# Performance work log

Measured on AMD Instinct MI355X. Metric: run time of the kernel, lower is better.

## Reference

```python
import jax, jax.numpy as jnp
import numpy as np

D = 768; H = 12; HEAD = 6; SD = 64; S1 = SD * (HEAD - 1); S2 = SD * HEAD
HID = 3072; B = 8; N = 1024
SCALE = (D // H) ** -0.5
EPS = 1e-5


def _ln(x, g, b):
    m = jnp.mean(x, axis=-1, keepdims=True)
    v = jnp.var(x, axis=-1, keepdims=True)
    return (x - m) * jax.lax.rsqrt(v + EPS) * g + b


def setup_inputs() -> dict:
    key = jax.random.key(0)
    ks = jax.random.split(key, 20)
    p = lambda k, shape, s=0.02: (jax.random.normal(k, shape, dtype=jnp.float32) * s)
    return {
        "x": jax.random.normal(ks[0], (B, N, D), dtype=jnp.float32),
        # norm1 / norm12 / norm13 (pre-attention split LayerNorms)
        "ln1a_g": jnp.ones((S1,), jnp.float32), "ln1a_b": jnp.zeros((S1,), jnp.float32),
        "ln1b_g": jnp.ones((SD,), jnp.float32), "ln1b_b": jnp.zeros((SD,), jnp.float32),
        "ln1c_g": jnp.ones((D - S2,), jnp.float32), "ln1c_b": jnp.zeros((D - S2,), jnp.float32),
        # norm2 / norm22 / norm23 (pre-MLP split LayerNorms)
        "ln2a_g": jnp.ones((S1,), jnp.float32), "ln2a_b": jnp.zeros((S1,), jnp.float32),
        "ln2b_g": jnp.ones((SD,), jnp.float32), "ln2b_b": jnp.zeros((SD,), jnp.float32),
        "ln2c_g": jnp.ones((D - S2,), jnp.float32), "ln2c_b": jnp.zeros((D - S2,), jnp.float32),
        # attention (qkv has no bias since qkv_bias=False)
        "qkv_w": p(ks[1], (3 * D, D)),
        "proj_w": p(ks[2], (D, D)), "proj_b": jnp.zeros((D,), jnp.float32),
        # mlp
        "fc1_w": p(ks[3], (HID, D)), "fc1_b": jnp.zeros((HID,), jnp.float32),
        "fc2_w": p(ks[4], (D, HID)), "fc2_b": jnp.zeros((D,), jnp.float32),
    }


def _split_norm(x, ga, ba, gb, bb, gc, bc):
    return jnp.concatenate([
        _ln(x[:, :, :S1], ga, ba),
        _ln(x[:, :, S1:S2], gb, bb),
        _ln(x[:, :, S2:], gc, bc),
    ], axis=2)


def _attention(x, qkv_w, proj_w, proj_b):
    Bq, Nq, C = x.shape
    hd = C // H
    qkv = jnp.einsum('bnc,dc->bnd', x, qkv_w)  # [B,N,3C]
    qkv = qkv.reshape(Bq, Nq, 3, H, hd).transpose(2, 0, 3, 1, 4)
    q, k, v = qkv[0], qkv[1], qkv[2]  # [B,H,N,hd]
    attn = jax.nn.softmax(jnp.einsum('bhqd,bhkd->bhqk', q, k) * SCALE, axis=-1)
    y = jnp.einsum('bhqk,bhkd->bhqd', attn, v)  # [B,H,N,hd]
    y = y.transpose(0, 2, 1, 3).reshape(Bq, Nq, C)
    return jnp.einsum('bnc,dc->bnd', y, proj_w) + proj_b


def reference(x, ln1a_g, ln1a_b, ln1b_g, ln1b_b, ln1c_g, ln1c_b,
              ln2a_g, ln2a_b, ln2b_g, ln2b_b, ln2c_g, ln2c_b,
              qkv_w, proj_w, proj_b, fc1_w, fc1_b, fc2_w, fc2_b):
    norm_x = _split_norm(x, ln1a_g, ln1a_b, ln1b_g, ln1b_b, ln1c_g, ln1c_b)
    x = x + _attention(norm_x, qkv_w, proj_w, proj_b)
    norm2_x = _split_norm(x, ln2a_g, ln2a_b, ln2b_g, ln2b_b, ln2c_g, ln2c_b)
    h = jax.nn.gelu(jnp.einsum('bnc,hc->bnh', norm2_x, fc1_w) + fc1_b, approximate=False)
    x = x + (jnp.einsum('bnh,ch->bnc', h, fc2_w) + fc2_b)
    return x
```

## Files before the change

### kernel.cpp

```cpp
#include <hip/hip_runtime.h>
#include <math.h>

#define NTOK 8192
#define DIM 768
#define SEQ 1024
#define NH 12
#define HD 64
#define HID 3072
#define S1V 320
#define S2V 384

typedef unsigned short bfu;
typedef __attribute__((ext_vector_type(8))) short short8;
typedef __attribute__((ext_vector_type(4))) float f32x4;

__device__ __forceinline__ bfu f2bf(float f){
  unsigned int u = __float_as_uint(f);
  u += 0x7FFFu + ((u >> 16) & 1u);
  return (bfu)(u >> 16);
}
__device__ __forceinline__ f32x4 mfma16(short8 a, short8 b, f32x4 c){
  return __builtin_amdgcn_mfma_f32_16x16x32_bf16(a, b, c, 0, 0, 0);
}
__device__ __forceinline__ void gll16(const void* g, void* l){
  __builtin_amdgcn_global_load_lds(
      (const __attribute__((address_space(1))) unsigned int*)g,
      (__attribute__((address_space(3))) unsigned int*)l, 16, 0, 0);
}
__device__ __forceinline__ int swz(int a){ return a ^ (((a >> 7) & 7) << 4); }

__global__ __launch_bounds__(256) void cvt_all(
    const float4* __restrict__ s0, ushort4* __restrict__ d0,
    const float4* __restrict__ s1, ushort4* __restrict__ d1,
    const float4* __restrict__ s2, ushort4* __restrict__ d2,
    const float4* __restrict__ s3, ushort4* __restrict__ d3)
{
  const int total = 1769472;
  for (int i = blockIdx.x * 256 + threadIdx.x; i < total; i += gridDim.x * 256){
    const float4* s; ushort4* d; int j = i;
    if (j < 442368)       { s = s0; d = d0; }
    else if (j < 589824)  { s = s1; d = d1; j -= 442368; }
    else if (j < 1179648) { s = s2; d = d2; j -= 589824; }
    else                  { s = s3; d = d3; j -= 1179648; }
    float4 f = s[j];
    ushort4 o;
    o.x = f2bf(f.x); o.y = f2bf(f.y); o.z = f2bf(f.z); o.w = f2bf(f.w);
    d[j] = o;
  }
}

__global__ __launch_bounds__(256) void ln_split(
    const float* __restrict__ x,
    const float* __restrict__ ga, const float* __restrict__ ba,
    const float* __restrict__ gb, const float* __restrict__ bb2,
    const float* __restrict__ gc, const float* __restrict__ bc,
    bfu* __restrict__ out)
{
  const int row = blockIdx.x, t = threadIdx.x;
  const float* xr = x + (size_t)row * DIM;
  const float e0 = xr[t], e1 = xr[t + 256], e2 = xr[t + 512];
  float s0 = e0, q0 = e0 * e0, s1 = 0.f, q1 = 0.f, s2 = e2, q2 = e2 * e2;
  const int i1 = t + 256;
  if (i1 < S1V)      { s0 += e1; q0 += e1 * e1; }
  else if (i1 < S2V) { s1 += e1; q1 += e1 * e1; }
  else               { s2 += e1; q2 += e1 * e1; }
  float v[6] = {s0, q0, s1, q1, s2, q2};
  #pragma unroll
  for (int k = 0; k < 6; ++k)
    #pragma unroll
    for (int off = 32; off; off >>= 1)
      v[k] += __shfl_xor(v[k], off);
  __shared__ float red[6][4];
  const int lane = t & 63, wave = t >> 6;
  if (lane == 0){
    #pragma unroll
    for (int k = 0; k < 6; ++k) red[k][wave] = v[k];
  }
  __syncthreads();
  float tt[6];
  #pragma unroll
  for (int k = 0; k < 6; ++k) tt[k] = red[k][0] + red[k][1] + red[k][2] + red[k][3];
  const float m0 = tt[0] * (1.f/320.f);
  const float r0 = rsqrtf(tt[1] * (1.f/320.f) - m0*m0 + 1e-5f);
  const float m1 = tt[2] * (1.f/64.f);
  const float r1 = rsqrtf(tt[3] * (1.f/64.f) - m1*m1 + 1e-5f);
  const float m2 = tt[4] * (1.f/384.f);
  const float r2 = rsqrtf(tt[5] * (1.f/384.f) - m2*m2 + 1e-5f);
  bfu* orow = out + (size_t)row * DIM;
  orow[t] = f2bf((e0 - m0) * r0 * ga[t] + ba[t]);
  {
    float ov;
    if (i1 < S1V)      ov = (e1 - m0) * r0 * ga[i1] + ba[i1];
    else if (i1 < S2V) ov = (e1 - m1) * r1 * gb[i1 - S1V] + bb2[i1 - S1V];
    else               ov = (e1 - m2) * r2 * gc[i1 - S2V] + bc[i1 - S2V];
    orow[i1] = f2bf(ov);
  }
  const int i2 = t + 512;
  orow[i2] = f2bf((e2 - m2) * r2 * gc[i2 - S2V] + bc[i2 - S2V]);
}

template<int FM, int FN, int BIAS, int GELU_, int RESID, int OUTF32, int QSC>
__device__ __forceinline__ void gemm_core(
    const bfu* __restrict__ A, const bfu* __restrict__ Bw,
    int N, int K, int ntn,
    const float* __restrict__ bias, const float* __restrict__ resid,
    float* __restrict__ outf, bfu* __restrict__ outb)
{
  constexpr int BM = FM * 32, BN = FN * 32;
  constexpr int ABYTES = BM * 64, BBYTES = BN * 64;
  constexpr int AISS = ABYTES / 4096, BISS = BBYTES / 4096;
  __shared__ __align__(16) char lA_[2][ABYTES];
  __shared__ __align__(16) char lB_[2][BBYTES];
  const int tid = threadIdx.x;
  const int lane = tid & 63;
  const int wave = tid >> 6;
  const int wm = wave >> 1, wn = wave & 1;
  const int r = lane & 15, g = lane >> 4;

  const int nwg = gridDim.x, cpx = nwg >> 3;
  const int sb = (blockIdx.x & 7) * cpx + (blockIdx.x >> 3);
  const int tm = sb / ntn, tn = sb % ntn;
  const size_t ld2 = (size_t)K * 2;

  f32x4 acc[FM][FN];
  #pragma unroll
  for (int i = 0; i < FM; ++i)
    #pragma unroll
    for (int j = 0; j < FN; ++j) acc[i][j] = (f32x4){0.f, 0.f, 0.f, 0.f};

  int PofA[AISS], rowA[AISS], colA[AISS];
  #pragma unroll
  for (int is = 0; is < AISS; ++is){
    const int P = is * 4096 + tid * 16, L = swz(P);
    PofA[is] = P; rowA[is] = L >> 6; colA[is] = L & 63;
  }
  int PofB[BISS], rowB[BISS], colB[BISS];
  #pragma unroll
  for (int is = 0; is < BISS; ++is){
    const int P = is * 4096 + tid * 16, L = swz(P);
    PofB[is] = P; rowB[is] = L >> 6; colB[is] = L & 63;
  }
  const char* Abase = (const char*)A + (size_t)tm * BM * ld2;
  const char* Bbase = (const char*)Bw + (size_t)tn * BN * ld2;

  int offA[FM], offB[FN];
  #pragma unroll
  for (int f = 0; f < FM; ++f) offA[f] = swz((wm * FM * 16 + f * 16 + r) * 64 + g * 16);
  #pragma unroll
  for (int f = 0; f < FN; ++f) offB[f] = swz((wn * FN * 16 + f * 16 + r) * 64 + g * 16);

  const int nk = K >> 5;
  #pragma unroll
  for (int is = 0; is < AISS; ++is)
    gll16(Abase + (size_t)rowA[is] * ld2 + colA[is], &lA_[0][PofA[is]]);
  #pragma unroll
  for (int is = 0; is < BISS; ++is)
    gll16(Bbase + (size_t)rowB[is] * ld2 + colB[is], &lB_[0][PofB[is]]);
  __syncthreads();

  for (int t = 0; t < nk; ++t){
    const int cur = t & 1;
    if (t + 1 < nk){
      const int kb = (t + 1) * 64;
      #pragma unroll
      for (int is = 0; is < AISS; ++is)
        gll16(Abase + (size_t)rowA[is] * ld2 + kb + colA[is], &lA_[cur ^ 1][PofA[is]]);
      #pragma unroll
      for (int is = 0; is < BISS; ++is)
        gll16(Bbase + (size_t)rowB[is] * ld2 + kb + colB[is], &lB_[cur ^ 1][PofB[is]]);
    }
    const char* lA = lA_[cur];
    const char* lB = lB_[cur];
    short8 af[FM], bf[FN];
    #pragma unroll
    for (int f = 0; f < FM; ++f) af[f] = *(const short8*)(lA + offA[f]);
    #pragma unroll
    for (int f = 0; f < FN; ++f) bf[f] = *(const short8*)(lB + offB[f]);
    #pragma unroll
    for (int i = 0; i < FM; ++i)
      #pragma unroll
      for (int j = 0; j < FN; ++j)
        acc[i][j] = mfma16(af[i], bf[j], acc[i][j]);
    __syncthreads();
  }

  const int row0 = tm * BM + wm * FM * 16;
  const int col0 = tn * BN + wn * FN * 16;
  #pragma unroll
  for (int j = 0; j < FN; ++j){
    const int colb = col0 + j * 16 + r;
    const float bi = BIAS ? bias[colb] : 0.f;
    #pragma unroll
    for (int i = 0; i < FM; ++i){
      #pragma unroll
      for (int q = 0; q < 4; ++q){
        const int rowg = row0 + i * 16 + g * 4 + q;
        float v = acc[i][j][q] + bi;
        if (GELU_) v = 0.5f * v * (1.f + erff(v * 0.70710678118654752440f));
        if (QSC && colb < 768) v *= 0.125f;
        const size_t idx = (size_t)rowg * N + colb;
        if (RESID) v += resid[idx];
        if (OUTF32) outf[idx] = v;
        else        outb[idx] = f2bf(v);
      }
    }
  }
}

__global__ __launch_bounds__(256) void gemm_qkv(const bfu* A, const bfu* Bw, bfu* out){
  gemm_core<4,4,0,0,0,0,1>(A, Bw, 2304, 768, 18, nullptr, nullptr, nullptr, out);
}
__global__ __launch_bounds__(256) void gemm_proj(const bfu* A, const bfu* Bw,
                                                 const float* bias, const float* resid, float* out){
  gemm_core<2,4,1,0,1,1,0>(A, Bw, 768, 768, 6, bias, resid, out, nullptr);
}
__global__ __launch_bounds__(256) void gemm_fc1(const bfu* A, const bfu* Bw,
                                                const float* bias, bfu* out){
  gemm_core<4,4,1,1,0,0,0>(A, Bw, 3072, 768, 24, bias, nullptr, nullptr, out);
}
__global__ __launch_bounds__(256) void gemm_fc2(const bfu* A, const bfu* Bw,
                                                const float* bias, float* out){
  gemm_core<2,4,1,0,1,1,0>(A, Bw, 768, 3072, 6, bias, out, out, nullptr);
}

__global__ __launch_bounds__(256) void vtrans(const bfu* __restrict__ qkv, bfu* __restrict__ vt){
  __shared__ bfu tile[64][66];
  const int bh = blockIdx.x, kt = blockIdx.y;
  const int b = bh / NH, h = bh - b * NH;
  const int tid = threadIdx.x;
  const int tr = tid >> 5;
  const int tc = (tid & 31) * 2;
  #pragma unroll
  for (int pass = 0; pass < 8; ++pass){
    const int k = pass * 8 + tr;
    const bfu* src = qkv + (size_t)(b * SEQ + kt * 64 + k) * 2304 + 1536 + h * 64 + tc;
    tile[k][tc] = src[0]; tile[k][tc + 1] = src[1];
  }
  __syncthreads();
  #pragma unroll
  for (int pass = 0; pass < 8; ++pass){
    const int d = pass * 8 + tr;
    bfu* dst = vt + ((size_t)bh * 64 + d) * SEQ + kt * 64 + tc;
    dst[0] = tile[tc][d]; dst[1] = tile[tc + 1][d];
  }
}

__global__ __launch_bounds__(512) void attn2(
    const bfu* __restrict__ qkv, const bfu* __restrict__ vt, bfu* __restrict__ y)
{
  __shared__ __align__(16) char kbuf[2][8192];
  __shared__ __align__(16) char vbuf[2][8192];
  __shared__ __align__(16) char plds_all[8][2048];
  const int tid = threadIdx.x, lane = tid & 63, wave = tid >> 6;
  char* plds = plds_all[wave];
  const int blk = blockIdx.x;
  const int bh = blk >> 3, q128 = blk & 7;
  const int b = bh / NH, h = bh - b * NH;
  const int r = lane & 15, g = lane >> 4;

  const bfu* qbase = qkv + (size_t)(b * SEQ + q128 * 128 + wave * 16 + r) * 2304 + h * 64;
  const short8 qf0 = *(const short8*)(qbase + g * 8);
  const short8 qf1 = *(const short8*)(qbase + 32 + g * 8);

  const int P = tid * 16;
  const int Ls = swz(P);
  const int srow = Ls >> 7, scol = Ls & 127;
  const char* kg = (const char*)(qkv + (size_t)(b * SEQ) * 2304 + 768 + h * 64)
                   + (size_t)srow * 4608 + scol;
  const char* vg = (const char*)(vt + (size_t)bh * 64 * SEQ)
                   + (size_t)srow * 2048 + scol;

  int off[4][2];
  #pragma unroll
  for (int f = 0; f < 4; ++f){
    off[f][0] = swz((f * 16 + r) * 128 + g * 16);
    off[f][1] = swz((f * 16 + r) * 128 + 64 + g * 16);
  }

  float m_[4], l_[4];
  f32x4 yacc[4];
  #pragma unroll
  for (int i = 0; i < 4; ++i){ m_[i] = -1e30f; l_[i] = 0.f; yacc[i] = (f32x4){0.f,0.f,0.f,0.f}; }

  gll16(kg, &kbuf[0][P]);
  gll16(vg, &vbuf[0][P]);
  __syncthreads();

  for (int kt = 0; kt < 16; ++kt){
    const int cur = kt & 1;
    if (kt + 1 < 16){
      gll16(kg + (size_t)(kt + 1) * 294912, &kbuf[cur ^ 1][P]);
      gll16(vg + (kt + 1) * 128, &vbuf[cur ^ 1][P]);
    }
    const char* lK = kbuf[cur];
    const char* lV = vbuf[cur];

    f32x4 s[4];
    #pragma unroll
    for (int c = 0; c < 4; ++c){
      const short8 kf0 = *(const short8*)(lK + off[c][0]);
      const short8 kf1 = *(const short8*)(lK + off[c][1]);
      s[c] = (f32x4){0.f, 0.f, 0.f, 0.f};
      s[c] = mfma16(qf0, kf0, s[c]);
      s[c] = mfma16(qf1, kf1, s[c]);
    }
    float pm[4];
    #pragma unroll
    for (int q = 0; q < 4; ++q)
      pm[q] = fmaxf(fmaxf(s[0][q], s[1][q]), fmaxf(s[2][q], s[3][q]));
    #pragma unroll
    for (int q = 0; q < 4; ++q)
      #pragma unroll
      for (int o = 1; o < 16; o <<= 1)
        pm[q] = fmaxf(pm[q], __shfl_xor(pm[q], o));
    float rs[4];
    #pragma unroll
    for (int q = 0; q < 4; ++q){
      const float mn = fmaxf(m_[q], pm[q]);
      const float al = __expf(m_[q] - mn);
      m_[q] = mn;
      l_[q] *= al;
      #pragma unroll
      for (int f = 0; f < 4; ++f) yacc[f][q] *= al;
      float acc = 0.f;
      #pragma unroll
      for (int c = 0; c < 4; ++c){
        const float p = __expf(s[c][q] - mn);
        s[c][q] = p;
        acc += p;
      }
      rs[q] = acc;
    }
    #pragma unroll
    for (int q = 0; q < 4; ++q){
      #pragma unroll
      for (int o = 1; o < 16; o <<= 1)
        rs[q] += __shfl_xor(rs[q], o);
      l_[q] += rs[q];
    }
    #pragma unroll
    for (int c = 0; c < 4; ++c)
      #pragma unroll
      for (int q = 0; q < 4; ++q){
        const int a = swz((g * 4 + q) * 128 + (c * 16 + r) * 2);
        *(bfu*)&plds[a] = f2bf(s[c][q]);
      }
    short8 pa[2];
    #pragma unroll
    for (int ks = 0; ks < 2; ++ks)
      pa[ks] = *(const short8*)&plds[swz(r * 128 + ks * 64 + g * 16)];
    #pragma unroll
    for (int f = 0; f < 4; ++f){
      const short8 vf0 = *(const short8*)(lV + off[f][0]);
      const short8 vf1 = *(const short8*)(lV + off[f][1]);
      yacc[f] = mfma16(pa[0], vf0, yacc[f]);
      yacc[f] = mfma16(pa[1], vf1, yacc[f]);
    }
    __syncthreads();
  }

  bfu* yb = y + (size_t)(b * SEQ + q128 * 128 + wave * 16) * DIM + h * 64;
  #pragma unroll
  for (int f = 0; f < 4; ++f)
    #pragma unroll
    for (int q = 0; q < 4; ++q)
      yb[(size_t)(g * 4 + q) * DIM + f * 16 + r] = f2bf(yacc[f][q] / l_[q]);
}

extern "C" void kernel_launch(void* const* d_in, const int* in_sizes, int n_in,
                              void* d_out, int out_size, void* d_ws, size_t ws_size,
                              hipStream_t stream) {
  const float* x      = (const float*)d_in[0];
  const float* ln1ag  = (const float*)d_in[1];
  const float* ln1ab  = (const float*)d_in[2];
  const float* ln1bg  = (const float*)d_in[3];
  const float* ln1bb  = (const float*)d_in[4];
  const float* ln1cg  = (const float*)d_in[5];
  const float* ln1cb  = (const float*)d_in[6];
  const float* ln2ag  = (const float*)d_in[7];
  const float* ln2ab  = (const float*)d_in[8];
  const float* ln2bg  = (const float*)d_in[9];
  const float* ln2bb  = (const float*)d_in[10];
  const float* ln2cg  = (const float*)d_in[11];
  const float* ln2cb  = (const float*)d_in[12];
  const float* qkv_w  = (const float*)d_in[13];
  const float* proj_w = (const float*)d_in[14];
  const float* proj_b = (const float*)d_in[15];
  const float* fc1_w  = (const float*)d_in[16];
  const float* fc1_b  = (const float*)d_in[17];
  const float* fc2_w  = (const float*)d_in[18];
  const float* fc2_b  = (const float*)d_in[19];
  float* outp = (float*)d_out;

  char* ws = (char*)d_ws;
  bfu* wqkv   = (bfu*)(ws + 0);
  bfu* wproj  = (bfu*)(ws + 3538944);
  bfu* wfc1   = (bfu*)(ws + 4718592);
  bfu* wfc2   = (bfu*)(ws + 9437184);
  bfu* lnbuf  = (bfu*)(ws + 14155776);
  bfu* ybuf   = (bfu*)(ws + 26738688);
  bfu* qkvbuf = (bfu*)(ws + 39321600);
  bfu* vtbuf  = (bfu*)(ws + 77070336);
  bfu* hbuf   = qkvbuf;

  cvt_all<<<2048, 256, 0, stream>>>((const float4*)qkv_w,  (ushort4*)wqkv,
                                    (const float4*)proj_w, (ushort4*)wproj,
                                    (const float4*)fc1_w,  (ushort4*)wfc1,
                                    (const float4*)fc2_w,  (ushort4*)wfc2);

  ln_split<<<NTOK, 256, 0, stream>>>(x, ln1ag, ln1ab, ln1bg, ln1bb, ln1cg, ln1cb, lnbuf);
  gemm_qkv<<<1152, 256, 0, stream>>>(lnbuf, wqkv, qkvbuf);
  vtrans<<<dim3(96,16), 256, 0, stream>>>(qkvbuf, vtbuf);
  attn2<<<768, 512, 0, stream>>>(qkvbuf, vtbuf, ybuf);
  gemm_proj<<<768, 256, 0, stream>>>(ybuf, wproj, proj_b, x, outp);
  ln_split<<<NTOK, 256, 0, stream>>>(outp, ln2ag, ln2ab, ln2bg, ln2bb, ln2cg, ln2cb, lnbuf);
  gemm_fc1<<<1536, 256, 0, stream>>>(lnbuf, wfc1, fc1_b, hbuf);
  gemm_fc2<<<768, 256, 0, stream>>>(hbuf, wfc2, fc2_b, outp);
}
```

Baseline: 457.0 us.

## Deepen GEMM K-tile to 64 with explicit vmcnt-based double-buffer prefetch

The GEMM core now stages 64-wide K tiles (128-byte rows) instead of 32-wide ones and issues loads two tiles ahead. Each wait uses a partial s_waitcnt vmcnt so the next tile's loads stay in flight while the current one is consumed, and the per-iteration __syncthreads is replaced by raw s_barrier. MFMA issue is bracketed with s_setprio and launch bounds ask for two blocks per CU. The aim is fewer barriers per unit of K and better overlap of global-to-LDS copies with matrix math. The cost is doubled LDS per stage and the risk that the hand-written vmcnt counts go wrong if the compiler reorders or adds memory ops.

```diff
diff --git a/kernel.cpp b/kernel.cpp
--- a/kernel.cpp
+++ b/kernel.cpp
@@ -99,18 +99,19 @@
   orow[i2] = f2bf((e2 - m2) * r2 * gc[i2 - S2V] + bc[i2 - S2V]);
 }
 
-template<int FM, int FN, int BIAS, int GELU_, int RESID, int OUTF32, int QSC>
-__device__ __forceinline__ void gemm_core(
+template<int BM, int BIAS, int GELU_, int RESID, int OUTF32, int QSC>
+__device__ __forceinline__ void gemm_core64(
     const bfu* __restrict__ A, const bfu* __restrict__ Bw,
     int N, int K, int ntn,
     const float* __restrict__ bias, const float* __restrict__ resid,
     float* __restrict__ outf, bfu* __restrict__ outb)
 {
-  constexpr int BM = FM * 32, BN = FN * 32;
-  constexpr int ABYTES = BM * 64, BBYTES = BN * 64;
-  constexpr int AISS = ABYTES / 4096, BISS = BBYTES / 4096;
-  __shared__ __align__(16) char lA_[2][ABYTES];
-  __shared__ __align__(16) char lB_[2][BBYTES];
+  constexpr int FM = BM / 32;
+  constexpr int AISS = BM / 32;
+  constexpr int BISS = 4;
+  constexpr int AB = AISS + BISS;
+  __shared__ __align__(16) char lA_[2][BM * 128];
+  __shared__ __align__(16) char lB_[2][128 * 128];
   const int tid = threadIdx.x;
   const int lane = tid & 63;
   const int wave = tid >> 6;
@@ -122,72 +123,89 @@
   const int tm = sb / ntn, tn = sb % ntn;
   const size_t ld2 = (size_t)K * 2;
 
-  f32x4 acc[FM][FN];
+  f32x4 acc[FM][4];
   #pragma unroll
   for (int i = 0; i < FM; ++i)
     #pragma unroll
-    for (int j = 0; j < FN; ++j) acc[i][j] = (f32x4){0.f, 0.f, 0.f, 0.f};
-
-  int PofA[AISS], rowA[AISS], colA[AISS];
-  #pragma unroll
-  for (int is = 0; is < AISS; ++is){
-    const int P = is * 4096 + tid * 16, L = swz(P);
-    PofA[is] = P; rowA[is] = L >> 6; colA[is] = L & 63;
-  }
-  int PofB[BISS], rowB[BISS], colB[BISS];
-  #pragma unroll
-  for (int is = 0; is < BISS; ++is){
-    const int P = is * 4096 + tid * 16, L = swz(P);
-    PofB[is] = P; rowB[is] = L >> 6; colB[is] = L & 63;
-  }
-  const char* Abase = (const char*)A + (size_t)tm * BM * ld2;
-  const char* Bbase = (const char*)Bw + (size_t)tn * BN * ld2;
-
-  int offA[FM], offB[FN];
-  #pragma unroll
-  for (int f = 0; f < FM; ++f) offA[f] = swz((wm * FM * 16 + f * 16 + r) * 64 + g * 16);
-  #pragma unroll
-  for (int f = 0; f < FN; ++f) offB[f] = swz((wn * FN * 16 + f * 16 + r) * 64 + g * 16);
-
-  const int nk = K >> 5;
-  #pragma unroll
-  for (int is = 0; is < AISS; ++is)
-    gll16(Abase + (size_t)rowA[is] * ld2 + colA[is], &lA_[0][PofA[is]]);
-  #pragma unroll
-  for (int is = 0; is < BISS; ++is)
-    gll16(Bbase + (size_t)rowB[is] * ld2 + colB[is], &lB_[0][PofB[is]]);
-  __syncthreads();
-
-  for (int t = 0; t < nk; ++t){
-    const int cur = t & 1;
-    if (t + 1 < nk){
-      const int kb = (t + 1) * 64;
-      #pragma unroll
-      for (int is = 0; is < AISS; ++is)
-        gll16(Abase + (size_t)rowA[is] * ld2 + kb + colA[is], &lA_[cur ^ 1][PofA[is]]);
-      #pragma unroll
-      for (int is = 0; is < BISS; ++is)
-        gll16(Bbase + (size_t)rowB[is] * ld2 + kb + colB[is], &lB_[cur ^ 1][PofB[is]]);
-    }
-    const char* lA = lA_[cur];
-    const char* lB = lB_[cur];
-    short8 af[FM], bf[FN];
-    #pragma unroll
-    for (int f = 0; f < FM; ++f) af[f] = *(const short8*)(lA + offA[f]);
-    #pragma unroll
-    for (int f = 0; f < FN; ++f) bf[f] = *(const short8*)(lB + offB[f]);
-    #pragma unroll
-    for (int i = 0; i < FM; ++i)
-      #pragma unroll
-      for (int j = 0; j < FN; ++j)
-        acc[i][j] = mfma16(af[i], bf[j], acc[i][j]);
-    __syncthreads();
-  }
-
-  const int row0 = tm * BM + wm * FM * 16;
-  const int col0 = tn * BN + wn * FN * 16;
-  #pragma unroll
-  for (int j = 0; j < FN; ++j){
+    for (int j = 0; j < 4; ++j) acc[i][j] = (f32x4){0.f, 0.f, 0.f, 0.f};
+
+  const int Ls = swz(tid * 16);
+  const int srow = Ls >> 7, scol = Ls & 127;
+  const char* Abase = (const char*)A + (size_t)tm * BM * ld2 + scol;
+  const char* Bbase = (const char*)Bw + (size_t)tn * 128 * ld2 + scol;
+  const int tid16 = tid * 16;
+  const int nt = K >> 6;
+
+  #define STG(slot, t) do { \
+    _Pragma("unroll") \
+    for (int is = 0; is < AISS; ++is) \
+      gll16(Abase + (size_t)(is * 32 + srow) * ld2 + (size_t)(t) * 128, \
+            &lA_[slot][is * 4096 + tid16]); \
+    _Pragma("unroll") \
+    for (int is = 0; is < BISS; ++is) \
+      gll16(Bbase + (size_t)(is * 32 + srow) * ld2 + (size_t)(t) * 128, \
+            &lB_[slot][is * 4096 + tid16]); \
+  } while (0)
+
+  int offA[FM][2], offB[4][2];
+  #pragma unroll
+  for (int f = 0; f < FM; ++f)
+    #pragma unroll
+    for (int h = 0; h < 2; ++h)
+      offA[f][h] = swz((wm * (BM / 2) + f * 16 + r) * 128 + h * 64 + g * 16);
+  #pragma unroll
+  for (int j = 0; j < 4; ++j)
+    #pragma unroll
+    for (int h = 0; h < 2; ++h)
+      offB[j][h] = swz((wn * 64 + j * 16 + r) * 128 + h * 64 + g * 16);
+
+  STG(0, 0);
+  STG(1, 1);
+
+  for (int t = 0; t < nt; ++t){
+    const int s = t & 1;
+    if (t + 1 < nt){
+      if constexpr (AB == 8) asm volatile("s_waitcnt vmcnt(8)" ::: "memory");
+      else                   asm volatile("s_waitcnt vmcnt(6)" ::: "memory");
+    } else {
+      asm volatile("s_waitcnt vmcnt(0)" ::: "memory");
+    }
+    __builtin_amdgcn_sched_barrier(0);
+    __builtin_amdgcn_s_barrier();
+
+    const char* lA = lA_[s];
+    const char* lB = lB_[s];
+    short8 af[FM][2], bf[4][2];
+    #pragma unroll
+    for (int f = 0; f < FM; ++f)
+      #pragma unroll
+      for (int h = 0; h < 2; ++h)
+        af[f][h] = *(const short8*)(lA + offA[f][h]);
+    #pragma unroll
+    for (int j = 0; j < 4; ++j)
+      #pragma unroll
+      for (int h = 0; h < 2; ++h)
+        bf[j][h] = *(const short8*)(lB + offB[j][h]);
+
+    __builtin_amdgcn_s_setprio(1);
+    #pragma unroll
+    for (int h = 0; h < 2; ++h)
+      #pragma unroll
+      for (int i = 0; i < FM; ++i)
+        #pragma unroll
+        for (int j = 0; j < 4; ++j)
+          acc[i][j] = mfma16(af[i][h], bf[j][h], acc[i][j]);
+    __builtin_amdgcn_s_setprio(0);
+
+    __builtin_amdgcn_s_barrier();
+    if (t + 2 < nt) STG(s, t + 2);
+  }
+  #undef STG
+
+  const int row0 = tm * BM + wm * (BM / 2);
+  const int col0 = tn * 128 + wn * 64;
+  #pragma unroll
+  for (int j = 0; j < 4; ++j){
     const int colb = col0 + j * 16 + r;
     const float bi = BIAS ? bias[colb] : 0.f;
     #pragma unroll
@@ -207,20 +225,20 @@
   }
 }
 
-__global__ __launch_bounds__(256) void gemm_qkv(const bfu* A, const bfu* Bw, bfu* out){
-  gemm_core<4,4,0,0,0,0,1>(A, Bw, 2304, 768, 18, nullptr, nullptr, nullptr, out);
-}
-__global__ __launch_bounds__(256) void gemm_proj(const bfu* A, const bfu* Bw,
-                                                 const float* bias, const float* resid, float* out){
-  gemm_core<2,4,1,0,1,1,0>(A, Bw, 768, 768, 6, bias, resid, out, nullptr);
-}
-__global__ __launch_bounds__(256) void gemm_fc1(const bfu* A, const bfu* Bw,
-                                                const float* bias, bfu* out){
-  gemm_core<4,4,1,1,0,0,0>(A, Bw, 3072, 768, 24, bias, nullptr, nullptr, out);
-}
-__global__ __launch_bounds__(256) void gemm_fc2(const bfu* A, const bfu* Bw,
-                                                const float* bias, float* out){
-  gemm_core<2,4,1,0,1,1,0>(A, Bw, 768, 3072, 6, bias, out, out, nullptr);
+__global__ __launch_bounds__(256, 2) void gemm_qkv(const bfu* A, const bfu* Bw, bfu* out){
+  gemm_core64<128,0,0,0,0,1>(A, Bw, 2304, 768, 18, nullptr, nullptr, nullptr, out);
+}
+__global__ __launch_bounds__(256, 2) void gemm_proj(const bfu* A, const bfu* Bw,
+                                                    const float* bias, const float* resid, float* out){
+  gemm_core64<64,1,0,1,1,0>(A, Bw, 768, 768, 6, bias, resid, out, nullptr);
+}
+__global__ __launch_bounds__(256, 2) void gemm_fc1(const bfu* A, const bfu* Bw,
+                                                   const float* bias, bfu* out){
+  gemm_core64<128,1,1,0,0,0>(A, Bw, 3072, 768, 24, bias, nullptr, nullptr, out);
+}
+__global__ __launch_bounds__(256, 2) void gemm_fc2(const bfu* A, const bfu* Bw,
+                                                   const float* bias, float* out){
+  gemm_core64<64,1,0,1,1,0>(A, Bw, 768, 3072, 6, bias, out, out, nullptr);
 }
 
 __global__ __launch_bounds__(256) void vtrans(const bfu* __restrict__ qkv, bfu* __restrict__ vt){
```

After: 409.6 us. 10.4% less time.
